# Optimization experiments

Hardware: AMD Instinct MI355X
Metric: run time of the kernel (lower is better)

The kernel has to match this reference:

```python
import jax, jax.numpy as jnp
import numpy as np

N_NODES = 20000
N_EDGES = 640000
HIDDEN = 128


def setup_inputs() -> dict:
    key = jax.random.key(0)
    k1, k2, k3, k4 = jax.random.split(key, 4)
    scale = 1.0 / np.sqrt(HIDDEN)
    features = jax.random.normal(k1, (N_NODES, HIDDEN), dtype=jnp.float32)
    edge_index = jax.random.randint(k2, (2, N_EDGES), 0, N_NODES, dtype=jnp.int64)
    W_l = jax.random.normal(k3, (HIDDEN, HIDDEN), dtype=jnp.float32) * scale
    b_l = jnp.zeros((HIDDEN,), dtype=jnp.float32)
    W_r = jax.random.normal(k4, (HIDDEN, HIDDEN), dtype=jnp.float32) * scale
    return {"features": features, "edge_index": edge_index, "W_l": W_l, "b_l": b_l, "W_r": W_r}


def reference(features, edge_index, W_l, b_l, W_r):
    # PyG SAGEConv with mean aggregation:
    #   out_i = lin_l(mean_{j : (j->i) in E} x_j) + lin_r(x_i)
    # edge_index[0] = source nodes, edge_index[1] = target nodes.
    n = features.shape[0]
    src = edge_index[0]
    dst = edge_index[1]
    msg = features[src]  # [E, d] gather
    summed = jax.ops.segment_sum(msg, dst, num_segments=n)  # [N, d] scatter-add
    cnt = jax.ops.segment_sum(jnp.ones(src.shape[0], dtype=features.dtype), dst, num_segments=n)
    agg = summed / jnp.maximum(cnt, 1.0)[:, None]  # mean; isolated nodes -> 0
    return agg @ W_l.T + b_l + features @ W_r.T
```

## Files before the change

### kernel.cpp

```cpp
#include <hip/hip_runtime.h>

#define N_NODES 20000
#define N_EDGES 640000
#define HIDDEN  128
#define CAP     96
#define DEG_PAD 16

typedef unsigned short bf16_t;
typedef __attribute__((ext_vector_type(8))) short short8;
typedef __attribute__((ext_vector_type(4))) float floatx4;

__device__ __forceinline__ bf16_t f2bf(float f) {
    union { float f; unsigned int i; } v; v.f = f;
    unsigned int x = v.i + 0x7FFFu + ((v.i >> 16) & 1u);
    return (bf16_t)(x >> 16);
}
__device__ __forceinline__ float bflo(unsigned u) {
    union { unsigned i; float f; } v; v.i = u << 16; return v.f;
}
__device__ __forceinline__ float bfhi(unsigned u) {
    union { unsigned i; float f; } v; v.i = u & 0xFFFF0000u; return v.f;
}

__global__ __launch_bounds__(256) void prep_fill_kernel(
        const float* __restrict__ feat,
        const float* __restrict__ Wl,
        const float* __restrict__ Wr,
        const int* __restrict__ eidx,
        bf16_t* __restrict__ feat_bf,
        bf16_t* __restrict__ Bp,
        int* __restrict__ deg,
        unsigned short* __restrict__ bucket) {
    int t = blockIdx.x * 256 + threadIdx.x;
    float4 v = ((const float4*)feat)[t];
    ushort4 o = { f2bf(v.x), f2bf(v.y), f2bf(v.z), f2bf(v.w) };
    ((ushort4*)feat_bf)[t] = o;
    int src = eidx[t];
    int dst = eidx[N_EDGES + t];
    int pos = atomicAdd(&deg[dst * DEG_PAD], 1);
    if (pos < CAP) bucket[dst * CAP + pos] = (unsigned short)src;
    if (t < 2 * HIDDEN * HIDDEN) {
        int j    = t & 7;
        int lane = (t >> 3) & 63;
        int nt   = (t >> 9) & 7;
        int kt   = t >> 12;
        int n = nt * 16 + (lane & 15);
        int k = kt * 32 + (lane >> 4) * 8 + j;
        float w = (k < HIDDEN) ? Wl[n * HIDDEN + k] : Wr[n * HIDDEN + (k - HIDDEN)];
        Bp[t] = f2bf(w);
    }
}

__global__ __launch_bounds__(256) void agg_kernel(
        const bf16_t* __restrict__ feat_bf,
        const int* __restrict__ deg,
        const unsigned short* __restrict__ bucket,
        bf16_t* __restrict__ agg) {
    int wid  = (blockIdx.x * 256 + threadIdx.x) >> 6;
    int lane = threadIdx.x & 63;
    if (wid >= N_NODES) return;
    int grp = lane >> 4;
    int c   = lane & 15;
    int d_true = deg[wid * DEG_PAD];
    int d = min(d_true, CAP);
    const unsigned short* row = bucket + (size_t)wid * CAP;
    const uint4* yq = (const uint4*)feat_bf;

    float a0=0,a1=0,a2=0,a3=0,a4=0,a5=0,a6=0,a7=0;
    int k = 0;
    for (; k + 16 <= d; k += 16) {
        int i0 = (int)row[k      + grp];
        int i1 = (int)row[k + 4  + grp];
        int i2 = (int)row[k + 8  + grp];
        int i3 = (int)row[k + 12 + grp];
        uint4 u0 = yq[i0 * 16 + c];
        uint4 u1 = yq[i1 * 16 + c];
        uint4 u2 = yq[i2 * 16 + c];
        uint4 u3 = yq[i3 * 16 + c];
        a0 += bflo(u0.x); a1 += bfhi(u0.x); a2 += bflo(u0.y); a3 += bfhi(u0.y);
        a4 += bflo(u0.z); a5 += bfhi(u0.z); a6 += bflo(u0.w); a7 += bfhi(u0.w);
        a0 += bflo(u1.x); a1 += bfhi(u1.x); a2 += bflo(u1.y); a3 += bfhi(u1.y);
        a4 += bflo(u1.z); a5 += bfhi(u1.z); a6 += bflo(u1.w); a7 += bfhi(u1.w);
        a0 += bflo(u2.x); a1 += bfhi(u2.x); a2 += bflo(u2.y); a3 += bfhi(u2.y);
        a4 += bflo(u2.z); a5 += bfhi(u2.z); a6 += bflo(u2.w); a7 += bfhi(u2.w);
        a0 += bflo(u3.x); a1 += bfhi(u3.x); a2 += bflo(u3.y); a3 += bfhi(u3.y);
        a4 += bflo(u3.z); a5 += bfhi(u3.z); a6 += bflo(u3.w); a7 += bfhi(u3.w);
    }
    for (; k < d; k += 4) {
        int kk = k + grp;
        int ia = (int)row[kk < d ? kk : (d - 1)];
        uint4 u = yq[ia * 16 + c];
        if (kk >= d) { u.x = 0u; u.y = 0u; u.z = 0u; u.w = 0u; }
        a0 += bflo(u.x); a1 += bfhi(u.x); a2 += bflo(u.y); a3 += bfhi(u.y);
        a4 += bflo(u.z); a5 += bfhi(u.z); a6 += bflo(u.w); a7 += bfhi(u.w);
    }
    a0 += __shfl_xor(a0, 16); a1 += __shfl_xor(a1, 16);
    a2 += __shfl_xor(a2, 16); a3 += __shfl_xor(a3, 16);
    a4 += __shfl_xor(a4, 16); a5 += __shfl_xor(a5, 16);
    a6 += __shfl_xor(a6, 16); a7 += __shfl_xor(a7, 16);
    a0 += __shfl_xor(a0, 32); a1 += __shfl_xor(a1, 32);
    a2 += __shfl_xor(a2, 32); a3 += __shfl_xor(a3, 32);
    a4 += __shfl_xor(a4, 32); a5 += __shfl_xor(a5, 32);
    a6 += __shfl_xor(a6, 32); a7 += __shfl_xor(a7, 32);
    if (grp == 0) {
        float inv = 1.0f / fmaxf((float)d_true, 1.0f);
        uint4 o;
        o.x = (unsigned)f2bf(a0 * inv) | ((unsigned)f2bf(a1 * inv) << 16);
        o.y = (unsigned)f2bf(a2 * inv) | ((unsigned)f2bf(a3 * inv) << 16);
        o.z = (unsigned)f2bf(a4 * inv) | ((unsigned)f2bf(a5 * inv) << 16);
        o.w = (unsigned)f2bf(a6 * inv) | ((unsigned)f2bf(a7 * inv) << 16);
        ((uint4*)agg)[wid * 16 + c] = o;
    }
}

__global__ __launch_bounds__(256) void gemm_out_kernel(
        const bf16_t* __restrict__ agg,
        const bf16_t* __restrict__ feat_bf,
        const bf16_t* __restrict__ Bp,
        const float* __restrict__ bl,
        float* __restrict__ out) {
    int wid = blockIdx.x * 4 + (threadIdx.x >> 6);
    if (wid >= N_NODES / 16) return;
    int lane = threadIdx.x & 63;
    int m    = lane & 15;
    int quad = lane >> 4;
    int row0 = wid * 16;

    floatx4 acc[8];
    floatx4 zf = {0.f, 0.f, 0.f, 0.f};
#pragma unroll
    for (int nt = 0; nt < 8; ++nt) acc[nt] = zf;

    const short8* bp = (const short8*)Bp;
#pragma unroll
    for (int kt = 0; kt < 8; ++kt) {
        const bf16_t* abase = (kt < 4)
            ? (agg     + (size_t)(row0 + m) * HIDDEN + kt * 32 + quad * 8)
            : (feat_bf + (size_t)(row0 + m) * HIDDEN + (kt - 4) * 32 + quad * 8);
        short8 afrag = *(const short8*)abase;
#pragma unroll
        for (int nt = 0; nt < 8; ++nt) {
            short8 bfrag = bp[(kt * 8 + nt) * 64 + lane];
            acc[nt] = __builtin_amdgcn_mfma_f32_16x16x32_bf16(afrag, bfrag, acc[nt], 0, 0, 0);
        }
    }
    int col = lane & 15;
#pragma unroll
    for (int nt = 0; nt < 8; ++nt) {
        float b = bl[nt * 16 + col];
#pragma unroll
        for (int r = 0; r < 4; ++r) {
            int row = row0 + quad * 4 + r;
            out[(size_t)row * HIDDEN + nt * 16 + col] = acc[nt][r] + b;
        }
    }
}

extern "C" void kernel_launch(void* const* d_in, const int* in_sizes, int n_in,
                              void* d_out, int out_size, void* d_ws, size_t ws_size,
                              hipStream_t stream) {
    const float* feat = (const float*)d_in[0];
    const int*   eidx = (const int*)d_in[1];
    const float* Wl   = (const float*)d_in[2];
    const float* bl   = (const float*)d_in[3];
    const float* Wr   = (const float*)d_in[4];
    float* out = (float*)d_out;

    int*            deg     = (int*)d_ws;
    unsigned short* bucket  = (unsigned short*)(deg + N_NODES * DEG_PAD);
    bf16_t*         Bp      = (bf16_t*)(bucket + (size_t)N_NODES * CAP);
    bf16_t*         feat_bf = Bp + 2 * HIDDEN * HIDDEN;
    bf16_t*         agg     = feat_bf + (size_t)N_NODES * HIDDEN;

    hipMemsetAsync(deg, 0, (size_t)N_NODES * DEG_PAD * sizeof(int), stream);

    prep_fill_kernel<<<N_EDGES / 256, 256, 0, stream>>>(
        feat, Wl, Wr, eidx, feat_bf, Bp, deg, bucket);
    agg_kernel<<<(N_NODES * 64) / 256, 256, 0, stream>>>(
        feat_bf, deg, bucket, agg);
    gemm_out_kernel<<<(N_NODES / 16 + 3) / 4, 256, 0, stream>>>(
        agg, feat_bf, Bp, bl, out);
}
```

Before: 130.5 us.

## Split neighbor aggregation into two feature-half passes for cache locality

The aggregation kernel is split into two launches, each gathering only 64 of the 128 bf16 feature columns, with 8 neighbor groups of 8 lanes per wave instead of 4 groups of 16. The intent is to halve the gathered working set per pass (2.5 MB per half) so random neighbor rows stay resident in L2/LLC. In exchange it adds a kernel launch, rereads the bucket and degree arrays twice, uses 64-byte rather than 256-byte contiguous segments per gathered row, and adds an extra shuffle reduction stage.

```diff
diff --git a/kernel.cpp b/kernel.cpp
--- a/kernel.cpp
+++ b/kernel.cpp
@@ -51,32 +51,34 @@
     }
 }
 
-__global__ __launch_bounds__(256) void agg_kernel(
+__global__ __launch_bounds__(256) void agg_half_kernel(
         const bf16_t* __restrict__ feat_bf,
         const int* __restrict__ deg,
         const unsigned short* __restrict__ bucket,
-        bf16_t* __restrict__ agg) {
+        bf16_t* __restrict__ agg,
+        int half) {
     int wid  = (blockIdx.x * 256 + threadIdx.x) >> 6;
     int lane = threadIdx.x & 63;
     if (wid >= N_NODES) return;
-    int grp = lane >> 4;
-    int c   = lane & 15;
+    int g = lane >> 3;
+    int c = lane & 7;
     int d_true = deg[wid * DEG_PAD];
     int d = min(d_true, CAP);
     const unsigned short* row = bucket + (size_t)wid * CAP;
     const uint4* yq = (const uint4*)feat_bf;
+    int hc = half * 8 + c;
 
     float a0=0,a1=0,a2=0,a3=0,a4=0,a5=0,a6=0,a7=0;
     int k = 0;
-    for (; k + 16 <= d; k += 16) {
-        int i0 = (int)row[k      + grp];
-        int i1 = (int)row[k + 4  + grp];
-        int i2 = (int)row[k + 8  + grp];
-        int i3 = (int)row[k + 12 + grp];
-        uint4 u0 = yq[i0 * 16 + c];
-        uint4 u1 = yq[i1 * 16 + c];
-        uint4 u2 = yq[i2 * 16 + c];
-        uint4 u3 = yq[i3 * 16 + c];
+    for (; k + 32 <= d; k += 32) {
+        int i0 = (int)row[k      + g];
+        int i1 = (int)row[k + 8  + g];
+        int i2 = (int)row[k + 16 + g];
+        int i3 = (int)row[k + 24 + g];
+        uint4 u0 = yq[i0 * 16 + hc];
+        uint4 u1 = yq[i1 * 16 + hc];
+        uint4 u2 = yq[i2 * 16 + hc];
+        uint4 u3 = yq[i3 * 16 + hc];
         a0 += bflo(u0.x); a1 += bfhi(u0.x); a2 += bflo(u0.y); a3 += bfhi(u0.y);
         a4 += bflo(u0.z); a5 += bfhi(u0.z); a6 += bflo(u0.w); a7 += bfhi(u0.w);
         a0 += bflo(u1.x); a1 += bfhi(u1.x); a2 += bflo(u1.y); a3 += bfhi(u1.y);
@@ -86,14 +88,28 @@
         a0 += bflo(u3.x); a1 += bfhi(u3.x); a2 += bflo(u3.y); a3 += bfhi(u3.y);
         a4 += bflo(u3.z); a5 += bfhi(u3.z); a6 += bflo(u3.w); a7 += bfhi(u3.w);
     }
-    for (; k < d; k += 4) {
-        int kk = k + grp;
+    for (; k + 16 <= d; k += 16) {
+        int i0 = (int)row[k     + g];
+        int i1 = (int)row[k + 8 + g];
+        uint4 u0 = yq[i0 * 16 + hc];
+        uint4 u1 = yq[i1 * 16 + hc];
+        a0 += bflo(u0.x); a1 += bfhi(u0.x); a2 += bflo(u0.y); a3 += bfhi(u0.y);
+        a4 += bflo(u0.z); a5 += bfhi(u0.z); a6 += bflo(u0.w); a7 += bfhi(u0.w);
+        a0 += bflo(u1.x); a1 += bfhi(u1.x); a2 += bflo(u1.y); a3 += bfhi(u1.y);
+        a4 += bflo(u1.z); a5 += bfhi(u1.z); a6 += bflo(u1.w); a7 += bfhi(u1.w);
+    }
+    for (; k < d; k += 8) {
+        int kk = k + g;
         int ia = (int)row[kk < d ? kk : (d - 1)];
-        uint4 u = yq[ia * 16 + c];
+        uint4 u = yq[ia * 16 + hc];
         if (kk >= d) { u.x = 0u; u.y = 0u; u.z = 0u; u.w = 0u; }
         a0 += bflo(u.x); a1 += bfhi(u.x); a2 += bflo(u.y); a3 += bfhi(u.y);
         a4 += bflo(u.z); a5 += bfhi(u.z); a6 += bflo(u.w); a7 += bfhi(u.w);
     }
+    a0 += __shfl_xor(a0, 8);  a1 += __shfl_xor(a1, 8);
+    a2 += __shfl_xor(a2, 8);  a3 += __shfl_xor(a3, 8);
+    a4 += __shfl_xor(a4, 8);  a5 += __shfl_xor(a5, 8);
+    a6 += __shfl_xor(a6, 8);  a7 += __shfl_xor(a7, 8);
     a0 += __shfl_xor(a0, 16); a1 += __shfl_xor(a1, 16);
     a2 += __shfl_xor(a2, 16); a3 += __shfl_xor(a3, 16);
     a4 += __shfl_xor(a4, 16); a5 += __shfl_xor(a5, 16);
@@ -102,14 +118,14 @@
     a2 += __shfl_xor(a2, 32); a3 += __shfl_xor(a3, 32);
     a4 += __shfl_xor(a4, 32); a5 += __shfl_xor(a5, 32);
     a6 += __shfl_xor(a6, 32); a7 += __shfl_xor(a7, 32);
-    if (grp == 0) {
+    if (g == 0) {
         float inv = 1.0f / fmaxf((float)d_true, 1.0f);
         uint4 o;
         o.x = (unsigned)f2bf(a0 * inv) | ((unsigned)f2bf(a1 * inv) << 16);
         o.y = (unsigned)f2bf(a2 * inv) | ((unsigned)f2bf(a3 * inv) << 16);
         o.z = (unsigned)f2bf(a4 * inv) | ((unsigned)f2bf(a5 * inv) << 16);
         o.w = (unsigned)f2bf(a6 * inv) | ((unsigned)f2bf(a7 * inv) << 16);
-        ((uint4*)agg)[wid * 16 + c] = o;
+        ((uint4*)agg)[wid * 16 + hc] = o;
     }
 }
 
@@ -176,8 +192,10 @@
 
     prep_fill_kernel<<<N_EDGES / 256, 256, 0, stream>>>(
         feat, Wl, Wr, eidx, feat_bf, Bp, deg, bucket);
-    agg_kernel<<<(N_NODES * 64) / 256, 256, 0, stream>>>(
-        feat_bf, deg, bucket, agg);
+    agg_half_kernel<<<(N_NODES * 64) / 256, 256, 0, stream>>>(
+        feat_bf, deg, bucket, agg, 0);
+    agg_half_kernel<<<(N_NODES * 64) / 256, 256, 0, stream>>>(
+        feat_bf, deg, bucket, agg, 1);
     gemm_out_kernel<<<(N_NODES / 16 + 3) / 4, 256, 0, stream>>>(
         agg, feat_bf, Bp, bl, out);
 }
```

New measurement: 138.8 us. 6.3% more time.
